# Performance work log

Hardware: AMD Instinct MI355X
Metric: run time of the kernel (lower is better)

## Reference

```python
import jax, jax.numpy as jnp
import numpy as np

K = 9          # top-k neighbors
GROUPS = 4     # GroupNorm groups
EPS_GN = 1e-5  # torch GroupNorm default eps


def group_norm(x, gamma, beta):
    # x: [B, C, H, W]; normalize over (C/GROUPS, H, W) per group
    B, C, H, W = x.shape
    xg = x.reshape(B, GROUPS, -1)
    mu = xg.mean(axis=-1, keepdims=True)
    var = xg.var(axis=-1, keepdims=True)
    xn = ((xg - mu) / jnp.sqrt(var + EPS_GN)).reshape(B, C, H, W)
    return xn * gamma[None, :, None, None] + beta[None, :, None, None]


def setup_inputs() -> dict:
    key = jax.random.key(0)
    ks = jax.random.split(key, 6)
    B, C, H, W = 32, 128, 45, 45
    std = 1.0 / np.sqrt(C)
    x = jax.random.normal(ks[0], (B, C, H, W), dtype=jnp.float32)
    w1 = jax.random.uniform(ks[1], (C, C), jnp.float32, -std, std)
    b1 = jax.random.uniform(ks[2], (C,), jnp.float32, -std, std)
    w2 = jax.random.uniform(ks[3], (C, C), jnp.float32, -std, std)
    b2 = jax.random.uniform(ks[4], (C,), jnp.float32, -std, std)
    gamma1 = jnp.ones((C,), jnp.float32)
    beta1 = jnp.zeros((C,), jnp.float32)
    gamma2 = jnp.ones((C,), jnp.float32)
    beta2 = jnp.zeros((C,), jnp.float32)
    return {"x": x, "w1": w1, "b1": b1, "w2": w2, "b2": b2,
            "gamma1": gamma1, "beta1": beta1, "gamma2": gamma2, "beta2": beta2}


def reference(x, w1, b1, w2, b2, gamma1, beta1, gamma2, beta2):
    B, C, H, W = x.shape
    N = H * W
    # build_knn: flatten, L2-normalize, cosine sim, top-k
    xf = x.reshape(B, C, N).transpose(0, 2, 1)                  # [B, N, C]
    nrm = jnp.linalg.norm(xf, axis=-1, keepdims=True)
    xn = xf / jnp.maximum(nrm, 1e-12)                           # F.normalize
    sim = jnp.einsum('bnc,bmc->bnm', xn, xn)                    # [B, N, N]
    val, idx = jax.lax.top_k(sim, K)                            # [B, N, K]
    # normalized edge weights (shared by both GCN layers)
    v = val / (val.sum(axis=-1, keepdims=True) + 1e-6)          # [B, N, K]

    def gcn_apply(feat, w, b):
        xt = feat @ w                                           # [B, N, C]
        neigh = jax.vmap(lambda t, i: t[i])(xt, idx)            # [B, N, K, C]
        return jnp.einsum('bnkc,bnk->bnc', neigh, v) + b

    out = gcn_apply(xn, w1, b1)
    out = jax.nn.silu(group_norm(out.transpose(0, 2, 1).reshape(B, C, H, W), gamma1, beta1))
    of = out.reshape(B, C, N).transpose(0, 2, 1)
    out = gcn_apply(of, w2, b2)
    out = jax.nn.silu(group_norm(out.transpose(0, 2, 1).reshape(B, C, H, W), gamma2, beta2))
    return out
```

## Files before the change

kernel.cpp:

```cpp
#include <hip/hip_runtime.h>
#include <hip/hip_bf16.h>

#define BN 32
#define CC 128
#define NN 2025
#define KK 9
#define NGROUP 4
#define CPG 32
#define GN_EPS 1e-5f
#define ROWS_TOTAL (BN * NN)

typedef _Float16 f16;
typedef __attribute__((ext_vector_type(8))) _Float16 f16x8;
typedef __attribute__((ext_vector_type(4))) float f32x4;

#define S28 3.725290298461914e-09f
#define S40 9.094947017729282e-13f
#define RH  6.103515625e-05f
#define RL  1.4901161193847656e-08f

#define T0F 0.17f
#define CAP 128

__global__ __launch_bounds__(256) void k_normalize(const float* __restrict__ x,
                                                   f16* __restrict__ xh, f16* __restrict__ xl) {
    int wid  = blockIdx.x * 4 + (threadIdx.x >> 6);
    int lane = threadIdx.x & 63;
    int b = wid / NN;
    int n = wid - b * NN;
    float v0 = x[(b * CC + lane) * NN + n];
    float v1 = x[(b * CC + lane + 64) * NN + n];
    float ss = v0 * v0 + v1 * v1;
#pragma unroll
    for (int off = 32; off > 0; off >>= 1) ss += __shfl_xor(ss, off);
    float s = 1.0f / fmaxf(sqrtf(ss), 1e-12f);
    v0 *= s; v1 *= s;
    float w0 = v0 * 16384.0f, w1 = v1 * 16384.0f;
    f16 h0 = (f16)w0, h1 = (f16)w1;
    f16 l0 = (f16)((w0 - (float)h0) * 4096.0f);
    f16 l1 = (f16)((w1 - (float)h1) * 4096.0f);
    size_t base = (size_t)wid * CC;
    xh[base + lane] = h0;  xh[base + lane + 64] = h1;
    xl[base + lane] = l0;  xl[base + lane + 64] = l1;
}

__device__ __forceinline__ void ins9(float cand, int m, float* v, int* ix,
                                     float& mv, int& mi, int& mp) {
    bool take = (cand > mv) || ((cand == mv) && (m < mi));
    if (take) {
#pragma unroll
        for (int k = 0; k < 9; ++k) if (k == mp) { v[k] = cand; ix[k] = m; }
        float nv = v[0]; int ni = ix[0]; int np = 0;
#pragma unroll
        for (int k = 1; k < 9; ++k) {
            if (v[k] < nv || (v[k] == nv && ix[k] > ni)) { nv = v[k]; ni = ix[k]; np = k; }
        }
        mv = nv; mi = ni; mp = np;
    }
}

__global__ __launch_bounds__(256) void k_sim_topk(const f16* __restrict__ xh, const f16* __restrict__ xl,
                                                  float* __restrict__ vout, int* __restrict__ iout) {
    __shared__ float sv[32][CAP];
    __shared__ int   si[32][CAP];
    __shared__ int   cnt[32];
    __shared__ int   nbad;
    __shared__ int   badrows[32];

    const int b    = blockIdx.y;
    const int r0   = blockIdx.x * 32;
    const int t    = threadIdx.x;
    const int w    = t >> 6;
    const int lane = t & 63;
    const int jr   = lane & 15;
    const int q    = lane >> 4;

    if (t < 32) cnt[t] = 0;
    if (t == 0) nbad = 0;

    f16x8 bh[2][4], bl[2][4];
#pragma unroll
    for (int tile = 0; tile < 2; ++tile) {
        int rr = b * NN + min(r0 + tile * 16 + jr, NN - 1);
        const f16* pH = xh + (size_t)rr * CC;
        const f16* pL = xl + (size_t)rr * CC;
#pragma unroll
        for (int s = 0; s < 4; ++s) {
            bh[tile][s] = *(const f16x8*)(pH + s * 32 + q * 8);
            bl[tile][s] = *(const f16x8*)(pL + s * 32 + q * 8);
        }
    }
    __syncthreads();

    for (int chunk = 0; chunk < 32; ++chunk) {
        const int mb = chunk * 64 + w * 16;
        const int marow = b * NN + min(mb + jr, NN - 1);
        const f16* aHp = xh + (size_t)marow * CC;
        const f16* aLp = xl + (size_t)marow * CC;
        f32x4 h0 = {0.f, 0.f, 0.f, 0.f}, l0 = {0.f, 0.f, 0.f, 0.f};
        f32x4 h1 = {0.f, 0.f, 0.f, 0.f}, l1 = {0.f, 0.f, 0.f, 0.f};
#pragma unroll
        for (int s = 0; s < 4; ++s) {
            f16x8 ah = *(const f16x8*)(aHp + s * 32 + q * 8);
            f16x8 al = *(const f16x8*)(aLp + s * 32 + q * 8);
            h0 = __builtin_amdgcn_mfma_f32_16x16x32_f16(ah, bh[0][s], h0, 0, 0, 0);
            l0 = __builtin_amdgcn_mfma_f32_16x16x32_f16(ah, bl[0][s], l0, 0, 0, 0);
            l0 = __builtin_amdgcn_mfma_f32_16x16x32_f16(al, bh[0][s], l0, 0, 0, 0);
            h1 = __builtin_amdgcn_mfma_f32_16x16x32_f16(ah, bh[1][s], h1, 0, 0, 0);
            l1 = __builtin_amdgcn_mfma_f32_16x16x32_f16(ah, bl[1][s], l1, 0, 0, 0);
            l1 = __builtin_amdgcn_mfma_f32_16x16x32_f16(al, bh[1][s], l1, 0, 0, 0);
        }
#pragma unroll
        for (int reg = 0; reg < 4; ++reg) {
            int m = mb + q * 4 + reg;
            float c0 = h0[reg] * S28 + l0[reg] * S40;
            if (m < NN && c0 > T0F) {
                int pos = atomicAdd(&cnt[jr], 1);
                if (pos < CAP) { sv[jr][pos] = c0; si[jr][pos] = m; }
            }
            float c1 = h1[reg] * S28 + l1[reg] * S40;
            if (m < NN && c1 > T0F) {
                int pos = atomicAdd(&cnt[16 + jr], 1);
                if (pos < CAP) { sv[16 + jr][pos] = c1; si[16 + jr][pos] = m; }
            }
        }
    }
    __syncthreads();

    if (t < 32) {
        int r = r0 + t;
        if (r < NN) {
            int c = cnt[t];
            if (c >= 9 && c <= CAP) {
                float fv[9]; int fi[9];
#pragma unroll
                for (int k = 0; k < 9; ++k) { fv[k] = -3.0e38f; fi[k] = 0x7fffffff; }
                float mv = -3.0e38f; int mi = 0x7fffffff; int mp = 0;
                for (int j = 0; j < c; ++j) ins9(sv[t][j], si[t][j], fv, fi, mv, mi, mp);
                float s = 1e-6f;
#pragma unroll
                for (int k = 0; k < 9; ++k) s += fv[k];
                float inv = 1.0f / s;
                int base = (b * NN + r) * KK;
#pragma unroll
                for (int k = 0; k < 9; ++k) { vout[base + k] = fv[k] * inv; iout[base + k] = fi[k]; }
            } else {
                int slot = atomicAdd(&nbad, 1);
                badrows[slot] = r;
            }
        }
    }
    __syncthreads();

    if (w == 0) {
        int nb = nbad;
        for (int ib = 0; ib < nb; ++ib) {
            int r = badrows[ib];
            const f16* rH = xh + ((size_t)b * NN + r) * CC;
            const f16* rL = xl + ((size_t)b * NN + r) * CC;
            float fv[9]; int fi[9];
#pragma unroll
            for (int k = 0; k < 9; ++k) { fv[k] = -3.0e38f; fi[k] = 0x7fffffff; }
            float mv = -3.0e38f; int mi = 0x7fffffff; int mp = 0;
            for (int m = lane; m < NN; m += 64) {
                const f16* mH = xh + ((size_t)b * NN + m) * CC;
                const f16* mL = xl + ((size_t)b * NN + m) * CC;
                float a1 = 0.f, a2 = 0.f;
                for (int c2 = 0; c2 < CC; ++c2) {
                    float hr = (float)rH[c2], hm = (float)mH[c2];
                    float lr = (float)rL[c2], lm = (float)mL[c2];
                    a1 += hr * hm;
                    a2 += hr * lm + lr * hm;
                }
                ins9(a1 * S28 + a2 * S40, m, fv, fi, mv, mi, mp);
            }
#pragma unroll
            for (int off = 1; off < 64; off <<= 1) {
                float pv[9]; int pi[9];
#pragma unroll
                for (int k = 0; k < 9; ++k) { pv[k] = __shfl_xor(fv[k], off); pi[k] = __shfl_xor(fi[k], off); }
#pragma unroll
                for (int k = 0; k < 9; ++k) ins9(pv[k], pi[k], fv, fi, mv, mi, mp);
            }
            if (lane == 0) {
                float s = 1e-6f;
#pragma unroll
                for (int k = 0; k < 9; ++k) s += fv[k];
                float inv = 1.0f / s;
                int base = (b * NN + r) * KK;
#pragma unroll
                for (int k = 0; k < 9; ++k) { vout[base + k] = fv[k] * inv; iout[base + k] = fi[k]; }
            }
        }
    }
}

#define RST 36
__global__ __launch_bounds__(256) void k_gemm_hl(const f16* __restrict__ xh, const f16* __restrict__ xl,
                                                 const float* __restrict__ w, float* __restrict__ out) {
    __shared__ float rowsT[CC * RST];
    int t = threadIdx.x;
    int row0 = blockIdx.x * 32;
    for (int it = 0; it < 16; ++it) {
        int qq = t + it * 256;
        int c = qq & 127, r = qq >> 7;
        size_t idx = (size_t)(row0 + r) * CC + c;
        rowsT[c * RST + r] = (float)xh[idx] * RH + (float)xl[idx] * RL;
    }
    __syncthreads();
    int j = t & 127, half = t >> 7;
    float acc[16];
#pragma unroll
    for (int r = 0; r < 16; ++r) acc[r] = 0.0f;
    for (int c = 0; c < CC; ++c) {
        float wv = w[c * CC + j];
        const float4* ap = (const float4*)&rowsT[c * RST + half * 16];
        float4 a0 = ap[0], a1 = ap[1], a2 = ap[2], a3 = ap[3];
        acc[0]  += a0.x * wv; acc[1]  += a0.y * wv; acc[2]  += a0.z * wv; acc[3]  += a0.w * wv;
        acc[4]  += a1.x * wv; acc[5]  += a1.y * wv; acc[6]  += a1.z * wv; acc[7]  += a1.w * wv;
        acc[8]  += a2.x * wv; acc[9]  += a2.y * wv; acc[10] += a2.z * wv; acc[11] += a2.w * wv;
        acc[12] += a3.x * wv; acc[13] += a3.y * wv; acc[14] += a3.z * wv; acc[15] += a3.w * wv;
    }
#pragma unroll
    for (int r = 0; r < 16; ++r) out[(size_t)(row0 + half * 16 + r) * CC + j] = acc[r];
}

__global__ __launch_bounds__(256) void k_gemm(const float* __restrict__ in,
                                              const float* __restrict__ w,
                                              float* __restrict__ out) {
    __shared__ float rowsT[CC * RST];
    int t = threadIdx.x;
    int row0 = blockIdx.x * 32;
    for (int it = 0; it < 16; ++it) {
        int qq = t + it * 256;
        int c = qq & 127, r = qq >> 7;
        rowsT[c * RST + r] = in[(size_t)(row0 + r) * CC + c];
    }
    __syncthreads();
    int j = t & 127, half = t >> 7;
    float acc[16];
#pragma unroll
    for (int r = 0; r < 16; ++r) acc[r] = 0.0f;
    for (int c = 0; c < CC; ++c) {
        float wv = w[c * CC + j];
        const float4* ap = (const float4*)&rowsT[c * RST + half * 16];
        float4 a0 = ap[0], a1 = ap[1], a2 = ap[2], a3 = ap[3];
        acc[0]  += a0.x * wv; acc[1]  += a0.y * wv; acc[2]  += a0.z * wv; acc[3]  += a0.w * wv;
        acc[4]  += a1.x * wv; acc[5]  += a1.y * wv; acc[6]  += a1.z * wv; acc[7]  += a1.w * wv;
        acc[8]  += a2.x * wv; acc[9]  += a2.y * wv; acc[10] += a2.z * wv; acc[11] += a2.w * wv;
        acc[12] += a3.x * wv; acc[13] += a3.y * wv; acc[14] += a3.z * wv; acc[15] += a3.w * wv;
    }
#pragma unroll
    for (int r = 0; r < 16; ++r) out[(size_t)(row0 + half * 16 + r) * CC + j] = acc[r];
}

__global__ __launch_bounds__(256) void k_gather(const float* __restrict__ xt,
                                                const float* __restrict__ v,
                                                const int* __restrict__ idx,
                                                const float* __restrict__ bias,
                                                float* __restrict__ out) {
    int t = threadIdx.x;
    int g = blockIdx.x * 2 + (t >> 7);
    int c = t & 127;
    if (g >= ROWS_TOTAL) return;
    int b = g / NN;
    int nb = b * NN;
    float acc = bias[c];
    int base = g * KK;
#pragma unroll
    for (int k = 0; k < KK; ++k) {
        int   ii = idx[base + k];
        float vv = v[base + k];
        acc += vv * xt[(size_t)(nb + ii) * CC + c];
    }
    out[(size_t)g * CC + c] = acc;
}

__global__ __launch_bounds__(256) void k_gnstats(const float* __restrict__ xin,
                                                 float* __restrict__ stats) {
    int bg = blockIdx.x; int b = bg >> 2; int gg = bg & 3;
    size_t base = (size_t)b * (NN * CC) + gg * CPG;
    float s1 = 0.f, s2 = 0.f;
    for (int i = threadIdx.x; i < NN * CPG; i += 256) {
        float x = xin[base + (size_t)(i >> 5) * CC + (i & 31)];
        s1 += x; s2 += x * x;
    }
#pragma unroll
    for (int off = 32; off > 0; off >>= 1) { s1 += __shfl_xor(s1, off); s2 += __shfl_xor(s2, off); }
    __shared__ float r1[4], r2[4];
    int w = threadIdx.x >> 6;
    if ((threadIdx.x & 63) == 0) { r1[w] = s1; r2[w] = s2; }
    __syncthreads();
    if (threadIdx.x == 0) {
        float a = r1[0] + r1[1] + r1[2] + r1[3];
        float qq = r2[0] + r2[1] + r2[2] + r2[3];
        const float inv = 1.0f / (float)(NN * CPG);
        float mean = a * inv;
        float var = qq * inv - mean * mean;
        stats[bg * 2]     = mean;
        stats[bg * 2 + 1] = rsqrtf(fmaxf(var, 0.f) + GN_EPS);
    }
}

__global__ __launch_bounds__(256) void k_gnsilu(const float* __restrict__ xin,
                                                const float* __restrict__ stats,
                                                const float* __restrict__ gamma,
                                                const float* __restrict__ beta,
                                                float* __restrict__ out) {
    size_t e4 = ((size_t)blockIdx.x * 256 + threadIdx.x) * 4;
    int c0 = (int)(e4 & 127);
    int b  = (int)(e4 / (NN * CC));
    int gg = c0 >> 5;
    float mean = stats[(b * 4 + gg) * 2];
    float rstd = stats[(b * 4 + gg) * 2 + 1];
    float4 x = *(const float4*)&xin[e4];
    float g0 = gamma[c0], g1 = gamma[c0 + 1], g2 = gamma[c0 + 2], g3 = gamma[c0 + 3];
    float p0 = beta[c0],  p1 = beta[c0 + 1],  p2 = beta[c0 + 2],  p3 = beta[c0 + 3];
    float y0 = (x.x - mean) * rstd * g0 + p0;
    float y1 = (x.y - mean) * rstd * g1 + p1;
    float y2 = (x.z - mean) * rstd * g2 + p2;
    float y3 = (x.w - mean) * rstd * g3 + p3;
    float4 r;
    r.x = y0 / (1.0f + expf(-y0));
    r.y = y1 / (1.0f + expf(-y1));
    r.z = y2 / (1.0f + expf(-y2));
    r.w = y3 / (1.0f + expf(-y3));
    *(float4*)&out[e4] = r;
}

__global__ __launch_bounds__(256) void k_gnsilu_out(const float* __restrict__ xin,
                                                    const float* __restrict__ stats,
                                                    const float* __restrict__ gamma,
                                                    const float* __restrict__ beta,
                                                    float* __restrict__ out) {
    __shared__ float tile[32 * 65];
    int b = blockIdx.z, ct = blockIdx.y, nt = blockIdx.x;
    int c0 = ct * 32, n0 = nt * 64;
    int t = threadIdx.x;
    int cj = t & 31, ni0 = t >> 5;
    int gg = c0 >> 5;
    float mean = stats[(b * 4 + gg) * 2];
    float rstd = stats[(b * 4 + gg) * 2 + 1];
    float gm = gamma[c0 + cj];
    float bt = beta[c0 + cj];
#pragma unroll
    for (int i = 0; i < 8; ++i) {
        int n = n0 + ni0 + i * 8;
        if (n < NN) {
            float x = xin[((size_t)b * NN + n) * CC + c0 + cj];
            float y = (x - mean) * rstd * gm + bt;
            y = y / (1.0f + expf(-y));
            tile[cj * 65 + ni0 + i * 8] = y;
        }
    }
    __syncthreads();
    int nj = t & 63, ci0 = t >> 6;
#pragma unroll
    for (int i = 0; i < 8; ++i) {
        int c = ci0 + i * 4;
        int n = n0 + nj;
        if (n < NN) out[((size_t)b * CC + c0 + c) * NN + n] = tile[c * 65 + nj];
    }
}

extern "C" void kernel_launch(void* const* d_in, const int* in_sizes, int n_in,
                              void* d_out, int out_size, void* d_ws, size_t ws_size,
                              hipStream_t stream) {
    const float* x      = (const float*)d_in[0];
    const float* w1     = (const float*)d_in[1];
    const float* b1     = (const float*)d_in[2];
    const float* w2     = (const float*)d_in[3];
    const float* b2     = (const float*)d_in[4];
    const float* gamma1 = (const float*)d_in[5];
    const float* beta1  = (const float*)d_in[6];
    const float* gamma2 = (const float*)d_in[7];
    const float* beta2  = (const float*)d_in[8];
    float* out = (float*)d_out;

    const size_t BIG = (size_t)ROWS_TOTAL * CC;
    float* ws   = (float*)d_ws;
    float* bufB = ws;
    f16*   xh   = (f16*)(ws + BIG);
    f16*   xl   = xh + BIG;
    float* bufA = ws + BIG;
    float* vbuf = ws + 2 * BIG;
    int*   ibuf = (int*)(ws + 2 * BIG + (size_t)ROWS_TOTAL * KK);
    float* stats = ws + 2 * BIG + 2 * (size_t)ROWS_TOTAL * KK;

    k_normalize<<<ROWS_TOTAL / 4, 256, 0, stream>>>(x, xh, xl);
    k_sim_topk<<<dim3(64, BN), 256, 0, stream>>>(xh, xl, vbuf, ibuf);

    k_gemm_hl<<<(ROWS_TOTAL + 31) / 32, 256, 0, stream>>>(xh, xl, w1, bufB);
    k_gather<<<ROWS_TOTAL / 2, 256, 0, stream>>>(bufB, vbuf, ibuf, b1, bufA);
    k_gnstats<<<BN * NGROUP, 256, 0, stream>>>(bufA, stats);
    k_gnsilu<<<(int)(BIG / 1024), 256, 0, stream>>>(bufA, stats, gamma1, beta1, bufB);

    k_gemm<<<(ROWS_TOTAL + 31) / 32, 256, 0, stream>>>(bufB, w2, bufA);
    k_gather<<<ROWS_TOTAL / 2, 256, 0, stream>>>(bufA, vbuf, ibuf, b2, bufB);
    k_gnstats<<<BN * NGROUP, 256, 0, stream>>>(bufB, stats);
    k_gnsilu_out<<<dim3((NN + 63) / 64, NGROUP, BN), 256, 0, stream>>>(bufB, stats, gamma2, beta2, out);
}
```

Baseline: 759.8 us.

## Replace threshold-candidate top-k with per-lane top-4 and separate exact fixup kernel

The similarity/top-k kernel no longer collects candidates above a fixed threshold into shared memory with atomics. Each lane now keeps a register top-4 per row segment, merges the segments to a top-9, and flags a row as bad only when some segment's fourth-best could still belong in the top-9. Bad rows go to a global list that a separate fixup kernel recomputes exactly, with the work spread across blocks. The normalize kernel is also rewritten to load a 64-row tile through shared memory with coalesced channel reads and to write f16x2 pairs. This removes the threshold heuristic and the serial fallback loop inside sim_topk, at the cost of an extra memset and kernel launch plus more register pressure.

```diff
diff --git a/kernel.cpp b/kernel.cpp
--- a/kernel.cpp
+++ b/kernel.cpp
@@ -9,8 +9,10 @@
 #define CPG 32
 #define GN_EPS 1e-5f
 #define ROWS_TOTAL (BN * NN)
+#define BADCAP 4096
 
 typedef _Float16 f16;
+typedef __attribute__((ext_vector_type(2))) _Float16 f16x2;
 typedef __attribute__((ext_vector_type(8))) _Float16 f16x8;
 typedef __attribute__((ext_vector_type(4))) float f32x4;
 
@@ -18,30 +20,48 @@
 #define S40 9.094947017729282e-13f
 #define RH  6.103515625e-05f
 #define RL  1.4901161193847656e-08f
-
-#define T0F 0.17f
-#define CAP 128
+#define NEG_INF -3.0e38f
 
 __global__ __launch_bounds__(256) void k_normalize(const float* __restrict__ x,
                                                    f16* __restrict__ xh, f16* __restrict__ xl) {
-    int wid  = blockIdx.x * 4 + (threadIdx.x >> 6);
-    int lane = threadIdx.x & 63;
-    int b = wid / NN;
-    int n = wid - b * NN;
-    float v0 = x[(b * CC + lane) * NN + n];
-    float v1 = x[(b * CC + lane + 64) * NN + n];
-    float ss = v0 * v0 + v1 * v1;
-#pragma unroll
-    for (int off = 32; off > 0; off >>= 1) ss += __shfl_xor(ss, off);
-    float s = 1.0f / fmaxf(sqrtf(ss), 1e-12f);
-    v0 *= s; v1 *= s;
-    float w0 = v0 * 16384.0f, w1 = v1 * 16384.0f;
-    f16 h0 = (f16)w0, h1 = (f16)w1;
-    f16 l0 = (f16)((w0 - (float)h0) * 4096.0f);
-    f16 l1 = (f16)((w1 - (float)h1) * 4096.0f);
-    size_t base = (size_t)wid * CC;
-    xh[base + lane] = h0;  xh[base + lane + 64] = h1;
-    xl[base + lane] = l0;  xl[base + lane + 64] = l1;
+    __shared__ float tile[64 * 129];
+    __shared__ float ssp[4][64];
+    __shared__ float invl[64];
+    int b = blockIdx.y, n0 = blockIdx.x * 64;
+    int t = threadIdx.x, w = t >> 6, l = t & 63;
+    const float* xb = x + (size_t)b * CC * NN;
+    int n = min(n0 + l, NN - 1);
+    float ss = 0.f;
+#pragma unroll 8
+    for (int cc = 0; cc < 32; ++cc) {
+        int c = w * 32 + cc;
+        float v = xb[(size_t)c * NN + n];
+        tile[l * 129 + c] = v;
+        ss += v * v;
+    }
+    ssp[w][l] = ss;
+    __syncthreads();
+    if (t < 64) {
+        float tot = ssp[0][t] + ssp[1][t] + ssp[2][t] + ssp[3][t];
+        invl[t] = 16384.0f / fmaxf(sqrtf(tot), 1e-12f);
+    }
+    __syncthreads();
+    size_t base = ((size_t)b * NN + n0) * CC;
+#pragma unroll 4
+    for (int j = 0; j < 16; ++j) {
+        int e2 = (j * 256 + t) * 2;
+        int nl2 = e2 >> 7, c2 = e2 & 127;
+        if (n0 + nl2 < NN) {
+            float inv = invl[nl2];
+            float a0 = tile[nl2 * 129 + c2] * inv;
+            float a1 = tile[nl2 * 129 + c2 + 1] * inv;
+            f16 h0 = (f16)a0, h1 = (f16)a1;
+            f16 lo0 = (f16)((a0 - (float)h0) * 4096.0f);
+            f16 lo1 = (f16)((a1 - (float)h1) * 4096.0f);
+            *(f16x2*)(xh + base + e2) = (f16x2){h0, h1};
+            *(f16x2*)(xl + base + e2) = (f16x2){lo0, lo1};
+        }
+    }
 }
 
 __device__ __forceinline__ void ins9(float cand, int m, float* v, int* ix,
@@ -59,13 +79,20 @@
     }
 }
 
+#define INS4(c, m, V, I)                                            \
+    {                                                               \
+        bool b0 = (c) > V[0], b1 = (c) > V[1], b2 = (c) > V[2], b3 = (c) > V[3]; \
+        V[3] = b3 ? (b2 ? V[2] : (c)) : V[3];  I[3] = b3 ? (b2 ? I[2] : (m)) : I[3]; \
+        V[2] = b2 ? (b1 ? V[1] : (c)) : V[2];  I[2] = b2 ? (b1 ? I[1] : (m)) : I[2]; \
+        V[1] = b1 ? (b0 ? V[0] : (c)) : V[1];  I[1] = b1 ? (b0 ? I[0] : (m)) : I[1]; \
+        V[0] = b0 ? (c) : V[0];                I[0] = b0 ? (m) : I[0]; \
+    }
+
 __global__ __launch_bounds__(256) void k_sim_topk(const f16* __restrict__ xh, const f16* __restrict__ xl,
-                                                  float* __restrict__ vout, int* __restrict__ iout) {
-    __shared__ float sv[32][CAP];
-    __shared__ int   si[32][CAP];
-    __shared__ int   cnt[32];
-    __shared__ int   nbad;
-    __shared__ int   badrows[32];
+                                                  float* __restrict__ vout, int* __restrict__ iout,
+                                                  int* __restrict__ badcnt, int* __restrict__ badlist) {
+    __shared__ float svf[32 * 16 * 4];
+    __shared__ int   sii[32 * 16 * 4];
 
     const int b    = blockIdx.y;
     const int r0   = blockIdx.x * 32;
@@ -75,9 +102,6 @@
     const int jr   = lane & 15;
     const int q    = lane >> 4;
 
-    if (t < 32) cnt[t] = 0;
-    if (t == 0) nbad = 0;
-
     f16x8 bh[2][4], bl[2][4];
 #pragma unroll
     for (int tile = 0; tile < 2; ++tile) {
@@ -90,7 +114,12 @@
             bl[tile][s] = *(const f16x8*)(pL + s * 32 + q * 8);
         }
     }
-    __syncthreads();
+
+    float sgv[2][4]; int sgi[2][4];
+#pragma unroll
+    for (int tile = 0; tile < 2; ++tile)
+#pragma unroll
+        for (int k = 0; k < 4; ++k) { sgv[tile][k] = NEG_INF; sgi[tile][k] = 0x7fffffff; }
 
     for (int chunk = 0; chunk < 32; ++chunk) {
         const int mb = chunk * 64 + w * 16;
@@ -113,30 +142,57 @@
 #pragma unroll
         for (int reg = 0; reg < 4; ++reg) {
             int m = mb + q * 4 + reg;
+            bool ok = (m < NN);
             float c0 = h0[reg] * S28 + l0[reg] * S40;
-            if (m < NN && c0 > T0F) {
-                int pos = atomicAdd(&cnt[jr], 1);
-                if (pos < CAP) { sv[jr][pos] = c0; si[jr][pos] = m; }
-            }
+            c0 = ok ? c0 : NEG_INF;
+            INS4(c0, m, sgv[0], sgi[0]);
             float c1 = h1[reg] * S28 + l1[reg] * S40;
-            if (m < NN && c1 > T0F) {
-                int pos = atomicAdd(&cnt[16 + jr], 1);
-                if (pos < CAP) { sv[16 + jr][pos] = c1; si[16 + jr][pos] = m; }
-            }
-        }
-    }
-    __syncthreads();
-
-    if (t < 32) {
-        int r = r0 + t;
-        if (r < NN) {
-            int c = cnt[t];
-            if (c >= 9 && c <= CAP) {
-                float fv[9]; int fi[9];
-#pragma unroll
-                for (int k = 0; k < 9; ++k) { fv[k] = -3.0e38f; fi[k] = 0x7fffffff; }
-                float mv = -3.0e38f; int mi = 0x7fffffff; int mp = 0;
-                for (int j = 0; j < c; ++j) ins9(sv[t][j], si[t][j], fv, fi, mv, mi, mp);
+            c1 = ok ? c1 : NEG_INF;
+            INS4(c1, m, sgv[1], sgi[1]);
+        }
+    }
+
+    int seg = w * 4 + q;
+#pragma unroll
+    for (int tile = 0; tile < 2; ++tile) {
+        int row = tile * 16 + jr;
+        int base = (row * 16 + seg) * 4;
+#pragma unroll
+        for (int k = 0; k < 4; ++k) { svf[base + k] = sgv[tile][k]; sii[base + k] = sgi[tile][k]; }
+    }
+    __syncthreads();
+
+    if (t < 64) {
+        int row = t & 31, half = t >> 5;
+        float fv[9]; int fi[9];
+#pragma unroll
+        for (int k = 0; k < 9; ++k) { fv[k] = NEG_INF; fi[k] = 0x7fffffff; }
+        float mv = NEG_INF; int mi = 0x7fffffff; int mp = 0;
+        for (int s = half * 8; s < half * 8 + 8; ++s) {
+            int base = (row * 16 + s) * 4;
+#pragma unroll
+            for (int k = 0; k < 4; ++k) ins9(svf[base + k], sii[base + k], fv, fi, mv, mi, mp);
+        }
+        float pv[9]; int pi[9];
+#pragma unroll
+        for (int k = 0; k < 9; ++k) { pv[k] = __shfl_xor(fv[k], 32); pi[k] = __shfl_xor(fi[k], 32); }
+#pragma unroll
+        for (int k = 0; k < 9; ++k) ins9(pv[k], pi[k], fv, fi, mv, mi, mp);
+
+        if (t < 32) {
+            int r = r0 + row;
+            if (r < NN) {
+                bool bad = false;
+#pragma unroll 4
+                for (int s = 0; s < 16; ++s) {
+                    float v3 = svf[(row * 16 + s) * 4 + 3];
+                    int   i3 = sii[(row * 16 + s) * 4 + 3];
+                    bad = bad || (v3 > mv) || (v3 == mv && i3 < mi);
+                }
+                if (bad) {
+                    int pos = atomicAdd(badcnt, 1);
+                    if (pos < BADCAP) badlist[pos] = (b << 12) | r;
+                }
                 float s = 1e-6f;
 #pragma unroll
                 for (int k = 0; k < 9; ++k) s += fv[k];
@@ -144,53 +200,64 @@
                 int base = (b * NN + r) * KK;
 #pragma unroll
                 for (int k = 0; k < 9; ++k) { vout[base + k] = fv[k] * inv; iout[base + k] = fi[k]; }
-            } else {
-                int slot = atomicAdd(&nbad, 1);
-                badrows[slot] = r;
             }
         }
     }
-    __syncthreads();
-
-    if (w == 0) {
-        int nb = nbad;
-        for (int ib = 0; ib < nb; ++ib) {
-            int r = badrows[ib];
-            const f16* rH = xh + ((size_t)b * NN + r) * CC;
-            const f16* rL = xl + ((size_t)b * NN + r) * CC;
-            float fv[9]; int fi[9];
-#pragma unroll
-            for (int k = 0; k < 9; ++k) { fv[k] = -3.0e38f; fi[k] = 0x7fffffff; }
-            float mv = -3.0e38f; int mi = 0x7fffffff; int mp = 0;
-            for (int m = lane; m < NN; m += 64) {
-                const f16* mH = xh + ((size_t)b * NN + m) * CC;
-                const f16* mL = xl + ((size_t)b * NN + m) * CC;
-                float a1 = 0.f, a2 = 0.f;
-                for (int c2 = 0; c2 < CC; ++c2) {
-                    float hr = (float)rH[c2], hm = (float)mH[c2];
-                    float lr = (float)rL[c2], lm = (float)mL[c2];
-                    a1 += hr * hm;
-                    a2 += hr * lm + lr * hm;
-                }
-                ins9(a1 * S28 + a2 * S40, m, fv, fi, mv, mi, mp);
+}
+
+__global__ __launch_bounds__(256) void k_topk_fix(const f16* __restrict__ xh, const f16* __restrict__ xl,
+                                                  const int* __restrict__ badcnt, const int* __restrict__ badlist,
+                                                  float* __restrict__ vout, int* __restrict__ iout) {
+    __shared__ float wvs[4][9];
+    __shared__ int   wis[4][9];
+    int nb = min(badcnt[0], BADCAP);
+    int t = threadIdx.x, w = t >> 6, lane = t & 63;
+    for (int i = blockIdx.x; i < nb; i += gridDim.x) {
+        __syncthreads();
+        int id = badlist[i];
+        int b = id >> 12, r = id & 4095;
+        const f16* rH = xh + ((size_t)b * NN + r) * CC;
+        const f16* rL = xl + ((size_t)b * NN + r) * CC;
+        float fv[9]; int fi[9];
+#pragma unroll
+        for (int k = 0; k < 9; ++k) { fv[k] = NEG_INF; fi[k] = 0x7fffffff; }
+        float mv = NEG_INF; int mi = 0x7fffffff; int mp = 0;
+        for (int m = t; m < NN; m += 256) {
+            const f16* mH = xh + ((size_t)b * NN + m) * CC;
+            const f16* mL = xl + ((size_t)b * NN + m) * CC;
+            float a1 = 0.f, a2 = 0.f;
+            for (int c = 0; c < CC; ++c) {
+                float hr = (float)rH[c], hm = (float)mH[c];
+                float lr = (float)rL[c], lm = (float)mL[c];
+                a1 += hr * hm;
+                a2 += hr * lm + lr * hm;
             }
-#pragma unroll
-            for (int off = 1; off < 64; off <<= 1) {
-                float pv[9]; int pi[9];
-#pragma unroll
-                for (int k = 0; k < 9; ++k) { pv[k] = __shfl_xor(fv[k], off); pi[k] = __shfl_xor(fi[k], off); }
-#pragma unroll
-                for (int k = 0; k < 9; ++k) ins9(pv[k], pi[k], fv, fi, mv, mi, mp);
-            }
-            if (lane == 0) {
-                float s = 1e-6f;
-#pragma unroll
-                for (int k = 0; k < 9; ++k) s += fv[k];
-                float inv = 1.0f / s;
-                int base = (b * NN + r) * KK;
-#pragma unroll
-                for (int k = 0; k < 9; ++k) { vout[base + k] = fv[k] * inv; iout[base + k] = fi[k]; }
-            }
+            ins9(a1 * S28 + a2 * S40, m, fv, fi, mv, mi, mp);
+        }
+#pragma unroll
+        for (int off = 1; off < 64; off <<= 1) {
+            float pv[9]; int pi[9];
+#pragma unroll
+            for (int k = 0; k < 9; ++k) { pv[k] = __shfl_xor(fv[k], off); pi[k] = __shfl_xor(fi[k], off); }
+#pragma unroll
+            for (int k = 0; k < 9; ++k) ins9(pv[k], pi[k], fv, fi, mv, mi, mp);
+        }
+        if (lane == 0) {
+#pragma unroll
+            for (int k = 0; k < 9; ++k) { wvs[w][k] = fv[k]; wis[w][k] = fi[k]; }
+        }
+        __syncthreads();
+        if (t == 0) {
+            for (int ww = 1; ww < 4; ++ww)
+#pragma unroll
+                for (int k = 0; k < 9; ++k) ins9(wvs[ww][k], wis[ww][k], fv, fi, mv, mi, mp);
+            float s = 1e-6f;
+#pragma unroll
+            for (int k = 0; k < 9; ++k) s += fv[k];
+            float inv = 1.0f / s;
+            int base = (b * NN + r) * KK;
+#pragma unroll
+            for (int k = 0; k < 9; ++k) { vout[base + k] = fv[k] * inv; iout[base + k] = fi[k]; }
         }
     }
 }
@@ -386,9 +453,14 @@
     float* vbuf = ws + 2 * BIG;
     int*   ibuf = (int*)(ws + 2 * BIG + (size_t)ROWS_TOTAL * KK);
     float* stats = ws + 2 * BIG + 2 * (size_t)ROWS_TOTAL * KK;
-
-    k_normalize<<<ROWS_TOTAL / 4, 256, 0, stream>>>(x, xh, xl);
-    k_sim_topk<<<dim3(64, BN), 256, 0, stream>>>(xh, xl, vbuf, ibuf);
+    int*   badcnt  = (int*)(stats + 256);
+    int*   badlist = badcnt + 1;
+
+    hipMemsetAsync(badcnt, 0, sizeof(int), stream);
+
+    k_normalize<<<dim3(32, BN), 256, 0, stream>>>(x, xh, xl);
+    k_sim_topk<<<dim3(64, BN), 256, 0, stream>>>(xh, xl, vbuf, ibuf, badcnt, badlist);
+    k_topk_fix<<<128, 256, 0, stream>>>(xh, xl, badcnt, badlist, vbuf, ibuf);
 
     k_gemm_hl<<<(ROWS_TOTAL + 31) / 32, 256, 0, stream>>>(xh, xl, w1, bufB);
     k_gather<<<ROWS_TOTAL / 2, 256, 0, stream>>>(bufB, vbuf, ibuf, b1, bufA);
```

New measurement: 1.545 ms. 103% more time.
